# Kernel optimization log

Measured on AMD Instinct MI355X. Metric: run time of the kernel, lower is better.

The kernel has to match this reference:

```python
import jax, jax.numpy as jnp
import numpy as np

N = 50000      # nodes
E = 800000     # edges (before self-loops)
IN = 128       # in_channels
HID = 16       # hidden_channels
HEADS = 8
OUT = 16       # out_channels
NEG_SLOPE = 0.2
BN_EPS = 1e-5
LN_EPS = 1e-5


def setup_inputs() -> dict:
    key = jax.random.key(0)
    ks = jax.random.split(key, 16)
    s = 0.05
    inp = {
        "x": jax.random.normal(ks[0], (N, IN), jnp.float32),
        "edge_index": jax.random.randint(ks[1], (2, E), 0, N, jnp.int64),
        # conv1 (in=IN, out=HID, heads=HEADS, concat=True)
        "Wl1": jax.random.normal(ks[2], (HEADS * HID, IN), jnp.float32) * s,
        "bl1": jnp.zeros((HEADS * HID,), jnp.float32),
        "Wr1": jax.random.normal(ks[3], (HEADS * HID, IN), jnp.float32) * s,
        "br1": jnp.zeros((HEADS * HID,), jnp.float32),
        "att1": jax.random.normal(ks[4], (HEADS, HID), jnp.float32) * s,
        "bias1": jnp.zeros((HEADS * HID,), jnp.float32),
        # batchnorm (eval mode, running stats)
        "bn_w": jnp.ones((HEADS * HID,), jnp.float32),
        "bn_b": jnp.zeros((HEADS * HID,), jnp.float32),
        "bn_rm": jnp.zeros((HEADS * HID,), jnp.float32),
        "bn_rv": jnp.ones((HEADS * HID,), jnp.float32),
        # conv2 (in=HEADS*HID, out=OUT, heads=HEADS, concat=False)
        "Wl2": jax.random.normal(ks[5], (HEADS * OUT, HEADS * HID), jnp.float32) * s,
        "bl2": jnp.zeros((HEADS * OUT,), jnp.float32),
        "Wr2": jax.random.normal(ks[6], (HEADS * OUT, HEADS * HID), jnp.float32) * s,
        "br2": jnp.zeros((HEADS * OUT,), jnp.float32),
        "att2": jax.random.normal(ks[7], (HEADS, OUT), jnp.float32) * s,
        "bias2": jnp.zeros((OUT,), jnp.float32),
        # skip + layernorm
        "Wskip": jax.random.normal(ks[8], (OUT, IN), jnp.float32) * s,
        "ln_w": jnp.ones((OUT,), jnp.float32),
        "ln_b": jnp.zeros((OUT,), jnp.float32),
    }
    return inp


def _gatv2(x, src, dst, Wl, bl, Wr, br, att, bias, heads, ch, concat):
    """PyG GATv2Conv (share_weights=False), eval mode (no dropout)."""
    n = x.shape[0]
    xl = (x @ Wl.T + bl).reshape(n, heads, ch)   # source transform
    xr = (x @ Wr.T + br).reshape(n, heads, ch)   # target transform
    # edge-wise attention score
    e = jax.nn.leaky_relu(xl[src] + xr[dst], NEG_SLOPE)          # [E',H,C]
    score = jnp.einsum('ehc,hc->eh', e, att)                      # [E',H]
    # segment softmax over incoming edges per destination node
    smax = jax.ops.segment_max(score, dst, num_segments=n)
    ex = jnp.exp(score - smax[dst])
    denom = jax.ops.segment_sum(ex, dst, num_segments=n)
    alpha = ex / denom[dst]                                       # [E',H]
    out = jax.ops.segment_sum(alpha[:, :, None] * xl[src], dst, num_segments=n)
    if concat:
        out = out.reshape(n, heads * ch)
    else:
        out = out.mean(axis=1)
    return out + bias


def reference(x, edge_index, Wl1, bl1, Wr1, br1, att1, bias1,
              bn_w, bn_b, bn_rm, bn_rv,
              Wl2, bl2, Wr2, br2, att2, bias2,
              Wskip, ln_w, ln_b):
    n = x.shape[0]
    loops = jnp.arange(n, dtype=edge_index.dtype)
    src = jnp.concatenate([edge_index[0], loops])
    dst = jnp.concatenate([edge_index[1], loops])

    x_res = x @ Wskip.T                                            # [N,OUT]

    h = _gatv2(x, src, dst, Wl1, bl1, Wr1, br1, att1, bias1, HEADS, HID, True)
    # BatchNorm1d in eval mode
    h = (h - bn_rm) * jax.lax.rsqrt(bn_rv + BN_EPS) * bn_w + bn_b
    h = jax.nn.elu(h)

    h = _gatv2(h, src, dst, Wl2, bl2, Wr2, br2, att2, bias2, HEADS, OUT, False)

    y = h + x_res
    mu = y.mean(axis=-1, keepdims=True)
    var = ((y - mu) ** 2).mean(axis=-1, keepdims=True)
    return (y - mu) * jax.lax.rsqrt(var + LN_EPS) * ln_w + ln_b
```

## Files before the change

### kernel.cpp

```cpp
#include <hip/hip_runtime.h>

#define NEG_SLOPE 0.2f
#define BN_EPS 1e-5f
#define LN_EPS 1e-5f

#if __has_builtin(__builtin_amdgcn_exp2f)
#define EXP2F(x) __builtin_amdgcn_exp2f(x)
#else
#define EXP2F(x) exp2f(x)
#endif

typedef __bf16 bf16_t;
typedef bf16_t bf16x8 __attribute__((ext_vector_type(8)));
typedef float floatx4 __attribute__((ext_vector_type(4)));

__device__ __forceinline__ unsigned short f2bf(float f) {
  unsigned u = __float_as_uint(f);
  u += 0x7FFFu + ((u >> 16) & 1u);
  return (unsigned short)(u >> 16);
}
__device__ __forceinline__ float bf_lo(unsigned u) { return __uint_as_float(u << 16); }
__device__ __forceinline__ float bf_hi(unsigned u) { return __uint_as_float(u & 0xFFFF0000u); }

__global__ void cvt_all(const float* __restrict__ wl1, const float* __restrict__ wr1,
                        const float* __restrict__ wl2, const float* __restrict__ wr2,
                        const float* __restrict__ wsk,
                        const float* __restrict__ bias1,
                        const float* __restrict__ bn_w, const float* __restrict__ bn_b,
                        const float* __restrict__ bn_rm, const float* __restrict__ bn_rv,
                        const int* __restrict__ ei, int E,
                        unsigned short* __restrict__ wcat1,
                        unsigned short* __restrict__ wcat2,
                        int* __restrict__ deg8, unsigned short* __restrict__ rpos,
                        float* __restrict__ bnS, float* __restrict__ bnT,
                        int N) {
  const int W4 = 128 * 128 / 4;
  const int S4 = 16 * 128 / 4;
  int j = blockIdx.x * blockDim.x + threadIdx.x;
  const float* src;
  unsigned short* dst;
  if (j < W4)               { src = wl1; dst = wcat1; }
  else if (j < 2 * W4)      { src = wr1; dst = wcat1 + 128 * 128; j -= W4; }
  else if (j < 3 * W4)      { src = wl2; dst = wcat2; j -= 2 * W4; }
  else if (j < 4 * W4)      { src = wr2; dst = wcat2 + 128 * 128; j -= 3 * W4; }
  else if (j < 4 * W4 + S4) { src = wsk; dst = wcat1 + 256 * 128; j -= 4 * W4; }
  else {
    j -= 4 * W4 + S4;
    if (j < 32) {
      for (int t = j * 4; t < j * 4 + 4; ++t) {
        float S = bn_w[t] * rsqrtf(bn_rv[t] + BN_EPS);
        bnS[t] = S;
        bnT[t] = (bias1[t] - bn_rm[t]) * S + bn_b[t];
      }
    } else {
      int e = j - 32;
      if (e < E) {
        int d = ei[E + e];
        int c = (int)(blockIdx.x & 7);
        rpos[e] = (unsigned short)atomicAdd(&deg8[(size_t)c * N + d], 1);
      }
    }
    return;
  }
  float4 v = ((const float4*)src)[j];
  ushort4 o;
  o.x = f2bf(v.x); o.y = f2bf(v.y); o.z = f2bf(v.z); o.w = f2bf(v.w);
  ((ushort4*)dst)[j] = o;
}

__global__ __launch_bounds__(1024)
void csr_scan(const int* __restrict__ deg8, int* __restrict__ meta,
              int* __restrict__ cbase8, int* bsum, int N) {
  __shared__ int wsum[16];
  __shared__ int sh_base;
  int b = blockIdx.x;
  int tid = threadIdx.x;
  int lane = tid & 63, wid = tid >> 6;
  int i0 = b * 4096 + tid * 4;

  int4 v[8];
#pragma unroll
  for (int c = 0; c < 8; ++c) {
    const int* p = deg8 + (size_t)c * N;
    v[c] = make_int4(0, 0, 0, 0);
    if (i0 + 3 < N) v[c] = *(const int4*)(p + i0);
    else if (i0 < N) {
      v[c].x = p[i0];
      if (i0 + 1 < N) v[c].y = p[i0 + 1];
      if (i0 + 2 < N) v[c].z = p[i0 + 2];
    }
  }
  int4 run = make_int4(0, 0, 0, 0);
#pragma unroll
  for (int c = 0; c < 8; ++c) {
    int4 t = v[c];
    v[c] = run;
    run.x += t.x; run.y += t.y; run.z += t.z; run.w += t.w;
  }
  int g1 = (run.x + 1) & ~1, g2 = (run.y + 1) & ~1, g3 = (run.z + 1) & ~1, g4 = (run.w + 1) & ~1;
  int s1 = g1, s2 = s1 + g2, s3 = s2 + g3, s4 = s3 + g4;
  int s = s4;
#pragma unroll
  for (int d = 1; d < 64; d <<= 1) { int t = __shfl_up(s, d, 64); if (lane >= d) s += t; }
  if (lane == 63) wsum[wid] = s;
  __syncthreads();
  if (tid < 16) {
    int ws = wsum[tid];
#pragma unroll
    for (int d = 1; d < 16; d <<= 1) { int t = __shfl_up(ws, d, 16); if (tid >= d) ws += t; }
    wsum[tid] = ws;
  }
  __syncthreads();
  if (tid == 0) {
    __hip_atomic_store(&bsum[b], wsum[15] + 1, __ATOMIC_RELEASE, __HIP_MEMORY_SCOPE_AGENT);
    int base = 0;
    for (int j = 0; j < b; ++j) {
      int x;
      do { x = __hip_atomic_load(&bsum[j], __ATOMIC_ACQUIRE, __HIP_MEMORY_SCOPE_AGENT); } while (x == 0);
      base += x - 1;
    }
    sh_base = base;
  }
  __syncthreads();
  int off = sh_base + (wid ? wsum[wid - 1] : 0) + (s - s4);
  int st[4] = {off, off + s1, off + s2, off + s3};
  int tv[4] = {run.x, run.y, run.z, run.w};
#pragma unroll
  for (int k = 0; k < 4; ++k)
    if (i0 + k < N) ((int2*)meta)[i0 + k] = make_int2(st[k], tv[k]);
#pragma unroll
  for (int c = 0; c < 8; ++c) {
    int* p = cbase8 + (size_t)c * N;
    if (i0 + 3 < N) {
      *(int4*)(p + i0) = make_int4(st[0] + v[c].x, st[1] + v[c].y, st[2] + v[c].z, st[3] + v[c].w);
    } else if (i0 < N) {
      p[i0] = st[0] + v[c].x;
      if (i0 + 1 < N) p[i0 + 1] = st[1] + v[c].y;
      if (i0 + 2 < N) p[i0 + 2] = st[2] + v[c].z;
    }
  }
}

template <bool MIXED, bool AF32>
__device__ __forceinline__ void gemm_body(int wv, int lane,
    const void* __restrict__ Av, const unsigned short* __restrict__ B,
    const float* __restrict__ bias0, const float* __restrict__ bias1,
    unsigned short* __restrict__ Cbf, float* __restrict__ Cf, int M, int pstrips) {
  int mtiles = (M + 31) >> 5;
  if (wv >= mtiles * 2) return;
  int mt = wv >> 1, sub = wv & 1;
  int r = lane & 15, quad = lane >> 4;

  bf16x8 a0[4], a1[4];
  if (AF32) {
    const float* Af = (const float*)Av;
    int r0 = min(mt * 32 + r, M - 1);
    int r1 = min(mt * 32 + 16 + r, M - 1);
    const float* A0 = Af + (size_t)r0 * 128 + quad * 8;
    const float* A1 = Af + (size_t)r1 * 128 + quad * 8;
#pragma unroll
    for (int k = 0; k < 4; ++k) {
      float4 fa = *(const float4*)(A0 + 32 * k);
      float4 fb = *(const float4*)(A0 + 32 * k + 4);
      float4 ga = *(const float4*)(A1 + 32 * k);
      float4 gb = *(const float4*)(A1 + 32 * k + 4);
      union { bf16x8 v; unsigned short s[8]; } t0, t1;
      t0.s[0] = f2bf(fa.x); t0.s[1] = f2bf(fa.y); t0.s[2] = f2bf(fa.z); t0.s[3] = f2bf(fa.w);
      t0.s[4] = f2bf(fb.x); t0.s[5] = f2bf(fb.y); t0.s[6] = f2bf(fb.z); t0.s[7] = f2bf(fb.w);
      t1.s[0] = f2bf(ga.x); t1.s[1] = f2bf(ga.y); t1.s[2] = f2bf(ga.z); t1.s[3] = f2bf(ga.w);
      t1.s[4] = f2bf(gb.x); t1.s[5] = f2bf(gb.y); t1.s[6] = f2bf(gb.z); t1.s[7] = f2bf(gb.w);
      a0[k] = t0.v;
      a1[k] = t1.v;
    }
  } else {
    const unsigned short* Au = (const unsigned short*)Av;
    const unsigned short* Abase = Au + (size_t)(mt * 32 + r) * 128 + quad * 8;
#pragma unroll
    for (int k = 0; k < 4; ++k) {
      a0[k] = *(const bf16x8*)(Abase + 32 * k);
      a1[k] = *(const bf16x8*)(Abase + 16 * 128 + 32 * k);
    }
  }

  int row0 = mt * 32 + quad * 4;
  const int Ptot = MIXED ? 272 : 256;
  for (int ps = sub; ps < pstrips; ps += 2) {
#pragma unroll
    for (int pp = 0; pp < 4; ++pp) {
      int p0 = ps * 64 + pp * 16;
      if (p0 >= Ptot) break;
      const unsigned short* Bbase = B + (size_t)(p0 + r) * 128 + quad * 8;
      bf16x8 b[4];
#pragma unroll
      for (int k = 0; k < 4; ++k) b[k] = *(const bf16x8*)(Bbase + 32 * k);
      floatx4 acc0 = {0.f, 0.f, 0.f, 0.f};
      floatx4 acc1 = {0.f, 0.f, 0.f, 0.f};
#pragma unroll
      for (int k = 0; k < 4; ++k) {
        acc0 = __builtin_amdgcn_mfma_f32_16x16x32_bf16(a0[k], b[k], acc0, 0, 0, 0);
        acc1 = __builtin_amdgcn_mfma_f32_16x16x32_bf16(a1[k], b[k], acc1, 0, 0, 0);
      }
      int col = p0 + r;
      if (MIXED && col >= 256) {
#pragma unroll
        for (int i = 0; i < 4; ++i) {
          if (row0 + i < M)      Cf[(size_t)(row0 + i) * 16 + (col - 256)] = acc0[i];
          if (row0 + 16 + i < M) Cf[(size_t)(row0 + 16 + i) * 16 + (col - 256)] = acc1[i];
        }
      } else {
        float bs = (col < 128) ? bias0[col] : bias1[col - 128];
#pragma unroll
        for (int i = 0; i < 4; ++i) {
          if (row0 + i < M)      Cbf[(size_t)(row0 + i) * 256 + col] = f2bf(acc0[i] + bs);
          if (row0 + 16 + i < M) Cbf[(size_t)(row0 + 16 + i) * 256 + col] = f2bf(acc1[i] + bs);
        }
      }
    }
  }
}

__global__ __launch_bounds__(256)
void gemm_bf16_mfma(const unsigned short* __restrict__ A, const unsigned short* __restrict__ B,
                    const float* __restrict__ bias0, const float* __restrict__ bias1,
                    unsigned short* __restrict__ Cbf, float* __restrict__ Cf,
                    int M, int pstrips) {
  gemm_body<false, false>((int)((blockIdx.x * blockDim.x + threadIdx.x) >> 6),
                          (int)(threadIdx.x & 63), A, B, bias0, bias1, Cbf, Cf, M, pstrips);
}

__global__ __launch_bounds__(256)
void gemm1_scatter(const float* __restrict__ A, const unsigned short* __restrict__ B,
                   const float* __restrict__ bias0, const float* __restrict__ bias1,
                   unsigned short* __restrict__ Cbf, float* __restrict__ Cf,
                   int M, int pstrips, int gemmBlocks,
                   const int* __restrict__ ei, int E, int ebase,
                   const int* __restrict__ cbase8, const unsigned short* __restrict__ rpos,
                   unsigned short* __restrict__ csr, int N) {
  if ((int)blockIdx.x >= gemmBlocks) {
    int e = ((int)blockIdx.x - gemmBlocks) * 256 + (int)threadIdx.x;
    if (e < E) {
      int d = ei[E + e];
      int c = ((ebase + e) >> 8) & 7;
      csr[cbase8[(size_t)c * N + d] + (int)rpos[e]] = (unsigned short)ei[e];
    }
    return;
  }
  gemm_body<true, true>((int)((blockIdx.x * blockDim.x + threadIdx.x) >> 6),
                        (int)(threadIdx.x & 63), A, B, bias0, bias1, Cbf, Cf, M, pstrips);
}

template <int LAYER>
__global__ __launch_bounds__(256)
void gat_agg(const unsigned int* __restrict__ xlr,
             const int* __restrict__ meta,
             const unsigned short* __restrict__ csr,
             const float* __restrict__ att,
             const float* __restrict__ p0, const float* __restrict__ p1,
             const float* __restrict__ p2, const float* __restrict__ p3,
             void* __restrict__ outp, int n, int nwaves) {
  int lane = threadIdx.x & 63;
  int gw = (int)((blockIdx.x * blockDim.x + threadIdx.x) >> 6);
  int slot = lane >> 4;
  int sl4 = lane & 15;
  const char* __restrict__ xb = (const char*)xlr;
  const unsigned slOff = (unsigned)(sl4 << 4);
  const int hsh = (slot & 1) << 4;
  const bool whi = (slot >= 2);
  float4 atA = ((const float4*)att)[sl4 * 2];
  float4 atB = ((const float4*)att)[sl4 * 2 + 1];
  const float SC = 0.6f * 1.44269504f;
  float a0 = SC * atA.x, a1 = SC * atA.y, a2 = SC * atA.z, a3 = SC * atA.w;
  float a4 = SC * atB.x, a5 = SC * atB.y, a6 = SC * atB.z, a7 = SC * atB.w;

  for (int dst = gw; dst < n; dst += nwaves) {
    int dsts = __builtin_amdgcn_readfirstlane(dst);
    int2 m = *(const int2*)(meta + 2 * (size_t)dsts);
    int beg = __builtin_amdgcn_readfirstlane(m.x);
    int dg  = __builtin_amdgcn_readfirstlane(m.y);
    const unsigned* cp = (const unsigned*)csr + (beg >> 1);

    uint4 urw = *(const uint4*)(xb + (((unsigned)dsts << 9) + 256u + slOff));
    float xr0 = bf_lo(urw.x), xr1 = bf_hi(urw.x), xr2 = bf_lo(urw.y), xr3 = bf_hi(urw.y);
    float xr4 = bf_lo(urw.z), xr5 = bf_hi(urw.z), xr6 = bf_lo(urw.w), xr7 = bf_hi(urw.w);

    float l = 0.f;
    float c0 = 0.f, c1 = 0.f, c2 = 0.f, c3 = 0.f;
    float c4 = 0.f, c5 = 0.f, c6 = 0.f, c7 = 0.f;

    auto gat = [&](unsigned w0, unsigned w1) -> uint4 {
      unsigned pr = whi ? w1 : w0;
      unsigned s = (pr >> hsh) & 0xFFFFu;
      return *(const uint4*)(xb + ((s << 9) + slOff));
    };

    auto body = [&](uint4 u, float vm, bool masked) {
      float x0 = bf_lo(u.x), x1 = bf_hi(u.x), x2 = bf_lo(u.y), x3 = bf_hi(u.y);
      float x4 = bf_lo(u.z), x5 = bf_hi(u.z), x6 = bf_lo(u.w), x7 = bf_hi(u.w);
      float e0 = x0 + xr0, e1 = x1 + xr1, e2 = x2 + xr2, e3 = x3 + xr3;
      float e4 = x4 + xr4, e5 = x5 + xr5, e6 = x6 + xr6, e7 = x7 + xr7;
      float sc = fmaf(fmaf(fabsf(e0), 0.66666667f, e0), a0,
                 fmaf(fmaf(fabsf(e1), 0.66666667f, e1), a1,
                 fmaf(fmaf(fabsf(e2), 0.66666667f, e2), a2,
                 fmaf(fmaf(fabsf(e3), 0.66666667f, e3), a3,
                 fmaf(fmaf(fabsf(e4), 0.66666667f, e4), a4,
                 fmaf(fmaf(fabsf(e5), 0.66666667f, e5), a5,
                 fmaf(fmaf(fabsf(e6), 0.66666667f, e6), a6,
                      fmaf(fabsf(e7), 0.66666667f, e7) * a7)))))));
      sc += __shfl_xor(sc, 1);
      float pw = EXP2F(sc);
      if (masked) pw *= vm;
      l += pw;
      c0 = fmaf(pw, x0, c0); c1 = fmaf(pw, x1, c1);
      c2 = fmaf(pw, x2, c2); c3 = fmaf(pw, x3, c3);
      c4 = fmaf(pw, x4, c4); c5 = fmaf(pw, x5, c5);
      c6 = fmaf(pw, x6, c6); c7 = fmaf(pw, x7, c7);
    };

    int nq = dg >> 2;
    int q = 0;
    int nq4 = nq & ~3;
    for (; q < nq4; q += 4) {
      unsigned w[8];
#pragma unroll
      for (int k = 0; k < 8; ++k) w[k] = cp[2 * q + k];
      uint4 u[4];
#pragma unroll
      for (int k = 0; k < 4; ++k) u[k] = gat(w[2 * k], w[2 * k + 1]);
#pragma unroll
      for (int k = 0; k < 4; ++k) body(u[k], 1.f, false);
    }
    if (nq - q >= 2) {
      unsigned w[4];
#pragma unroll
      for (int k = 0; k < 4; ++k) w[k] = cp[2 * q + k];
      uint4 u[2];
#pragma unroll
      for (int k = 0; k < 2; ++k) u[k] = gat(w[2 * k], w[2 * k + 1]);
#pragma unroll
      for (int k = 0; k < 2; ++k) body(u[k], 1.f, false);
      q += 2;
    }
    if (nq - q >= 1) {
      unsigned w0 = cp[2 * q], w1 = cp[2 * q + 1];
      body(gat(w0, w1), 1.f, false);
      q += 1;
    }
    {
      unsigned w0 = cp[2 * q], w1 = cp[2 * q + 1];
      int tot = dg + 1;
      int e = 4 * q + slot;
      unsigned pr = whi ? w1 : w0;
      unsigned sE = (pr >> hsh) & 0xFFFFu;
      unsigned s = (e < dg) ? sE : (unsigned)dsts;
      float vm = (e < tot) ? 1.f : 0.f;
      uint4 u = *(const uint4*)(xb + ((s << 9) + slOff));
      body(u, vm, true);
    }

    l  += __shfl_xor(l, 16);  l  += __shfl_xor(l, 32);
    c0 += __shfl_xor(c0, 16); c0 += __shfl_xor(c0, 32);
    c1 += __shfl_xor(c1, 16); c1 += __shfl_xor(c1, 32);
    c2 += __shfl_xor(c2, 16); c2 += __shfl_xor(c2, 32);
    c3 += __shfl_xor(c3, 16); c3 += __shfl_xor(c3, 32);
    c4 += __shfl_xor(c4, 16); c4 += __shfl_xor(c4, 32);
    c5 += __shfl_xor(c5, 16); c5 += __shfl_xor(c5, 32);
    c6 += __shfl_xor(c6, 16); c6 += __shfl_xor(c6, 32);
    c7 += __shfl_xor(c7, 16); c7 += __shfl_xor(c7, 32);
    float inv = 1.f / l;

    if (LAYER == 1) {
      float4 Sa = *(const float4*)(p0 + sl4 * 8);
      float4 Sb = *(const float4*)(p0 + sl4 * 8 + 4);
      float4 Ta = *(const float4*)(p1 + sl4 * 8);
      float4 Tb = *(const float4*)(p1 + sl4 * 8 + 4);
      float o0 = fmaf(c0 * inv, Sa.x, Ta.x);
      float o1 = fmaf(c1 * inv, Sa.y, Ta.y);
      float o2 = fmaf(c2 * inv, Sa.z, Ta.z);
      float o3 = fmaf(c3 * inv, Sa.w, Ta.w);
      float o4 = fmaf(c4 * inv, Sb.x, Tb.x);
      float o5 = fmaf(c5 * inv, Sb.y, Tb.y);
      float o6 = fmaf(c6 * inv, Sb.z, Tb.z);
      float o7 = fmaf(c7 * inv, Sb.w, Tb.w);
      o0 = (o0 > 0.f) ? o0 : (__expf(o0) - 1.f);
      o1 = (o1 > 0.f) ? o1 : (__expf(o1) - 1.f);
      o2 = (o2 > 0.f) ? o2 : (__expf(o2) - 1.f);
      o3 = (o3 > 0.f) ? o3 : (__expf(o3) - 1.f);
      o4 = (o4 > 0.f) ? o4 : (__expf(o4) - 1.f);
      o5 = (o5 > 0.f) ? o5 : (__expf(o5) - 1.f);
      o6 = (o6 > 0.f) ? o6 : (__expf(o6) - 1.f);
      o7 = (o7 > 0.f) ? o7 : (__expf(o7) - 1.f);
      if (slot == 0) {
        uint4 o;
        o.x = ((unsigned)f2bf(o1) << 16) | f2bf(o0);
        o.y = ((unsigned)f2bf(o3) << 16) | f2bf(o2);
        o.z = ((unsigned)f2bf(o5) << 16) | f2bf(o4);
        o.w = ((unsigned)f2bf(o7) << 16) | f2bf(o6);
        ((uint4*)outp)[(size_t)dsts * 16 + sl4] = o;
      }
    } else {
      float y0 = c0 * inv, y1 = c1 * inv, y2 = c2 * inv, y3 = c3 * inv;
      float y4 = c4 * inv, y5 = c5 * inv, y6 = c6 * inv, y7 = c7 * inv;
#pragma unroll
      for (int d = 2; d <= 8; d <<= 1) {
        y0 += __shfl_xor(y0, d); y1 += __shfl_xor(y1, d);
        y2 += __shfl_xor(y2, d); y3 += __shfl_xor(y3, d);
        y4 += __shfl_xor(y4, d); y5 += __shfl_xor(y5, d);
        y6 += __shfl_xor(y6, d); y7 += __shfl_xor(y7, d);
      }
      int chh = (sl4 & 1) * 8;
      float4 b2a = *(const float4*)(p1 + chh);
      float4 b2b = *(const float4*)(p1 + chh + 4);
      float4 xsa = *(const float4*)(p0 + (size_t)dsts * 16 + chh);
      float4 xsb = *(const float4*)(p0 + (size_t)dsts * 16 + chh + 4);
      y0 = y0 * 0.125f + b2a.x + xsa.x;
      y1 = y1 * 0.125f + b2a.y + xsa.y;
      y2 = y2 * 0.125f + b2a.z + xsa.z;
      y3 = y3 * 0.125f + b2a.w + xsa.w;
      y4 = y4 * 0.125f + b2b.x + xsb.x;
      y5 = y5 * 0.125f + b2b.y + xsb.y;
      y6 = y6 * 0.125f + b2b.z + xsb.z;
      y7 = y7 * 0.125f + b2b.w + xsb.w;
      float t = ((y0 + y1) + (y2 + y3)) + ((y4 + y5) + (y6 + y7));
      t += __shfl_xor(t, 1);
      float mu = t * (1.f / 16.f);
      float d0 = y0 - mu, d1 = y1 - mu, d2 = y2 - mu, d3 = y3 - mu;
      float d4 = y4 - mu, d5 = y5 - mu, d6 = y6 - mu, d7 = y7 - mu;
      float v = ((d0 * d0 + d1 * d1) + (d2 * d2 + d3 * d3)) +
                ((d4 * d4 + d5 * d5) + (d6 * d6 + d7 * d7));
      v += __shfl_xor(v, 1);
      float istd = rsqrtf(v * (1.f / 16.f) + LN_EPS);
      float4 lwa = *(const float4*)(p2 + chh);
      float4 lwb = *(const float4*)(p2 + chh + 4);
      float4 lba = *(const float4*)(p3 + chh);
      float4 lbb = *(const float4*)(p3 + chh + 4);
      if (lane < 2) {
        float4 oa, ob;
        oa.x = d0 * istd * lwa.x + lba.x;
        oa.y = d1 * istd * lwa.y + lba.y;
        oa.z = d2 * istd * lwa.z + lba.z;
        oa.w = d3 * istd * lwa.w + lba.w;
        ob.x = d4 * istd * lwb.x + lbb.x;
        ob.y = d5 * istd * lwb.y + lbb.y;
        ob.z = d6 * istd * lwb.z + lbb.z;
        ob.w = d7 * istd * lwb.w + lbb.w;
        float* op = (float*)outp + (size_t)dsts * 16 + chh;
        *(float4*)op = oa;
        *(float4*)(op + 4) = ob;
      }
    }
  }
}

extern "C" void kernel_launch(void* const* d_in, const int* in_sizes, int n_in,
                              void* d_out, int out_size, void* d_ws, size_t ws_size,
                              hipStream_t stream) {
  const float* x     = (const float*)d_in[0];
  const int*   ei    = (const int*)d_in[1];
  const float* Wl1   = (const float*)d_in[2];
  const float* bl1   = (const float*)d_in[3];
  const float* Wr1   = (const float*)d_in[4];
  const float* br1   = (const float*)d_in[5];
  const float* att1  = (const float*)d_in[6];
  const float* bias1 = (const float*)d_in[7];
  const float* bn_w  = (const float*)d_in[8];
  const float* bn_b  = (const float*)d_in[9];
  const float* bn_rm = (const float*)d_in[10];
  const float* bn_rv = (const float*)d_in[11];
  const float* Wl2   = (const float*)d_in[12];
  const float* bl2   = (const float*)d_in[13];
  const float* Wr2   = (const float*)d_in[14];
  const float* br2   = (const float*)d_in[15];
  const float* att2  = (const float*)d_in[16];
  const float* bias2 = (const float*)d_in[17];
  const float* Wskip = (const float*)d_in[18];
  const float* ln_w  = (const float*)d_in[19];
  const float* ln_b  = (const float*)d_in[20];

  const int N = in_sizes[0] / 128;
  const int E = in_sizes[1] / 2;

  char* w = (char*)d_ws;
  size_t off = 0;
  auto alloc = [&](size_t bytes) -> void* {
    void* p = (void*)(w + off);
    off += (bytes + 255) & ~(size_t)255;
    return p;
  };
  unsigned short* wcat1  = (unsigned short*)alloc(272 * 128 * 2);
  unsigned short* wcat2  = (unsigned short*)alloc(256 * 128 * 2);
  unsigned int*   xlr    = (unsigned int*)alloc((size_t)N * 128 * 4);
  float*          xres   = (float*)alloc((size_t)N * 16 * 4);
  unsigned short* hbf    = (unsigned short*)alloc((size_t)N * 128 * 2);
  float*          bnS    = (float*)alloc(128 * 4);
  float*          bnT    = (float*)alloc(128 * 4);
  int*            deg8   = (int*)alloc((size_t)8 * N * 4);
  int*            bsum   = (int*)alloc(64 * 4);
  int*            cbase8 = (int*)alloc((size_t)8 * N * 4);
  int*            meta   = (int*)alloc((size_t)2 * N * 4);
  unsigned short* rpos   = (unsigned short*)alloc((size_t)E * 2);
  unsigned short* csr    = (unsigned short*)alloc((size_t)(E + N) * 2 + 256);

  const int W4 = 128 * 128 / 4, S4 = 16 * 128 / 4;
  const int ebase = 4 * W4 + S4 + 32;
  const int nb = (N + 4095) / 4096;

  hipMemsetAsync(deg8, 0, (size_t)8 * N * 4 + 256 + 64 * 4, stream);
  {
    int tot = ebase + E;
    cvt_all<<<(tot + 255) / 256, 256, 0, stream>>>(
        Wl1, Wr1, Wl2, Wr2, Wskip, bias1, bn_w, bn_b, bn_rm, bn_rv, ei, E,
        wcat1, wcat2, deg8, rpos, bnS, bnT, N);
  }

  csr_scan<<<nb, 1024, 0, stream>>>(deg8, meta, cbase8, bsum, N);

  {
    int mtiles = (N + 31) >> 5;
    int waves = mtiles * 2;
    int gemmBlocks = (waves + 3) / 4;
    int scatBlocks = (E + 255) / 256;
    gemm1_scatter<<<gemmBlocks + scatBlocks, 256, 0, stream>>>(
        x, wcat1, bl1, br1, (unsigned short*)xlr, xres, N, 5, gemmBlocks,
        ei, E, ebase, cbase8, rpos, csr, N);
  }

  {
    int blocks = 6144, nwaves = blocks * 4;
    gat_agg<1><<<blocks, 256, 0, stream>>>(xlr, meta, csr, att1,
                                           bnS, bnT, nullptr, nullptr, (void*)hbf, N, nwaves);
  }

  {
    int mtiles = (N + 31) >> 5;
    int waves = mtiles * 2;
    gemm_bf16_mfma<<<(waves + 3) / 4, 256, 0, stream>>>(
        hbf, wcat2, bl2, br2, (unsigned short*)xlr, nullptr, N, 4);
  }

  {
    int blocks = 6144, nwaves = blocks * 4;
    gat_agg<2><<<blocks, 256, 0, stream>>>(xlr, meta, csr, att2,
                                           xres, bias2, ln_w, ln_b, d_out, N, nwaves);
  }
}
```

Measured before the change: 301.3 us.

## Split interleaved xl/xr buffer into separate arrays and shrink aggregation grid

The GEMM outputs for the source (xl) and target (xr) transforms move out of one interleaved 512-byte-per-node row into two separate 256-byte-per-node arrays. The aggregation kernels gather only xl rows, so the gathered table is denser, which should make better use of cache. The aggregation launch also drops from 6144 to 2048 blocks, so each wave handles more destination nodes in its grid-stride loop.

```diff
diff --git a/kernel.cpp b/kernel.cpp
--- a/kernel.cpp
+++ b/kernel.cpp
@@ -145,7 +145,8 @@
 __device__ __forceinline__ void gemm_body(int wv, int lane,
     const void* __restrict__ Av, const unsigned short* __restrict__ B,
     const float* __restrict__ bias0, const float* __restrict__ bias1,
-    unsigned short* __restrict__ Cbf, float* __restrict__ Cf, int M, int pstrips) {
+    unsigned short* __restrict__ Cl, unsigned short* __restrict__ Cr,
+    float* __restrict__ Cf, int M, int pstrips) {
   int mtiles = (M + 31) >> 5;
   if (wv >= mtiles * 2) return;
   int mt = wv >> 1, sub = wv & 1;
@@ -209,10 +210,12 @@
         }
       } else {
         float bs = (col < 128) ? bias0[col] : bias1[col - 128];
+        unsigned short* Ct = (col < 128) ? Cl : Cr;
+        int cc = col & 127;
 #pragma unroll
         for (int i = 0; i < 4; ++i) {
-          if (row0 + i < M)      Cbf[(size_t)(row0 + i) * 256 + col] = f2bf(acc0[i] + bs);
-          if (row0 + 16 + i < M) Cbf[(size_t)(row0 + 16 + i) * 256 + col] = f2bf(acc1[i] + bs);
+          if (row0 + i < M)      Ct[(size_t)(row0 + i) * 128 + cc] = f2bf(acc0[i] + bs);
+          if (row0 + 16 + i < M) Ct[(size_t)(row0 + 16 + i) * 128 + cc] = f2bf(acc1[i] + bs);
         }
       }
     }
@@ -222,16 +225,18 @@
 __global__ __launch_bounds__(256)
 void gemm_bf16_mfma(const unsigned short* __restrict__ A, const unsigned short* __restrict__ B,
                     const float* __restrict__ bias0, const float* __restrict__ bias1,
-                    unsigned short* __restrict__ Cbf, float* __restrict__ Cf,
+                    unsigned short* __restrict__ Cl, unsigned short* __restrict__ Cr,
                     int M, int pstrips) {
   gemm_body<false, false>((int)((blockIdx.x * blockDim.x + threadIdx.x) >> 6),
-                          (int)(threadIdx.x & 63), A, B, bias0, bias1, Cbf, Cf, M, pstrips);
+                          (int)(threadIdx.x & 63), A, B, bias0, bias1, Cl, Cr, nullptr,
+                          M, pstrips);
 }
 
 __global__ __launch_bounds__(256)
 void gemm1_scatter(const float* __restrict__ A, const unsigned short* __restrict__ B,
                    const float* __restrict__ bias0, const float* __restrict__ bias1,
-                   unsigned short* __restrict__ Cbf, float* __restrict__ Cf,
+                   unsigned short* __restrict__ Cl, unsigned short* __restrict__ Cr,
+                   float* __restrict__ Cf,
                    int M, int pstrips, int gemmBlocks,
                    const int* __restrict__ ei, int E, int ebase,
                    const int* __restrict__ cbase8, const unsigned short* __restrict__ rpos,
@@ -246,12 +251,13 @@
     return;
   }
   gemm_body<true, true>((int)((blockIdx.x * blockDim.x + threadIdx.x) >> 6),
-                        (int)(threadIdx.x & 63), A, B, bias0, bias1, Cbf, Cf, M, pstrips);
+                        (int)(threadIdx.x & 63), A, B, bias0, bias1, Cl, Cr, Cf, M, pstrips);
 }
 
 template <int LAYER>
 __global__ __launch_bounds__(256)
-void gat_agg(const unsigned int* __restrict__ xlr,
+void gat_agg(const unsigned short* __restrict__ xlt,
+             const unsigned short* __restrict__ xrt,
              const int* __restrict__ meta,
              const unsigned short* __restrict__ csr,
              const float* __restrict__ att,
@@ -262,7 +268,7 @@
   int gw = (int)((blockIdx.x * blockDim.x + threadIdx.x) >> 6);
   int slot = lane >> 4;
   int sl4 = lane & 15;
-  const char* __restrict__ xb = (const char*)xlr;
+  const char* __restrict__ xb = (const char*)xlt;
   const unsigned slOff = (unsigned)(sl4 << 4);
   const int hsh = (slot & 1) << 4;
   const bool whi = (slot >= 2);
@@ -279,7 +285,7 @@
     int dg  = __builtin_amdgcn_readfirstlane(m.y);
     const unsigned* cp = (const unsigned*)csr + (beg >> 1);
 
-    uint4 urw = *(const uint4*)(xb + (((unsigned)dsts << 9) + 256u + slOff));
+    uint4 urw = *(const uint4*)((const char*)xrt + (((unsigned)dsts << 8) + slOff));
     float xr0 = bf_lo(urw.x), xr1 = bf_hi(urw.x), xr2 = bf_lo(urw.y), xr3 = bf_hi(urw.y);
     float xr4 = bf_lo(urw.z), xr5 = bf_hi(urw.z), xr6 = bf_lo(urw.w), xr7 = bf_hi(urw.w);
 
@@ -290,7 +296,7 @@
     auto gat = [&](unsigned w0, unsigned w1) -> uint4 {
       unsigned pr = whi ? w1 : w0;
       unsigned s = (pr >> hsh) & 0xFFFFu;
-      return *(const uint4*)(xb + ((s << 9) + slOff));
+      return *(const uint4*)(xb + ((s << 8) + slOff));
     };
 
     auto body = [&](uint4 u, float vm, bool masked) {
@@ -353,7 +359,7 @@
       unsigned sE = (pr >> hsh) & 0xFFFFu;
       unsigned s = (e < dg) ? sE : (unsigned)dsts;
       float vm = (e < tot) ? 1.f : 0.f;
-      uint4 u = *(const uint4*)(xb + ((s << 9) + slOff));
+      uint4 u = *(const uint4*)(xb + ((s << 8) + slOff));
       body(u, vm, true);
     }
 
@@ -488,7 +494,8 @@
   };
   unsigned short* wcat1  = (unsigned short*)alloc(272 * 128 * 2);
   unsigned short* wcat2  = (unsigned short*)alloc(256 * 128 * 2);
-  unsigned int*   xlr    = (unsigned int*)alloc((size_t)N * 128 * 4);
+  unsigned short* xlt    = (unsigned short*)alloc((size_t)N * 128 * 2);
+  unsigned short* xrt    = (unsigned short*)alloc((size_t)N * 128 * 2);
   float*          xres   = (float*)alloc((size_t)N * 16 * 4);
   unsigned short* hbf    = (unsigned short*)alloc((size_t)N * 128 * 2);
   float*          bnS    = (float*)alloc(128 * 4);
@@ -520,13 +527,13 @@
     int gemmBlocks = (waves + 3) / 4;
     int scatBlocks = (E + 255) / 256;
     gemm1_scatter<<<gemmBlocks + scatBlocks, 256, 0, stream>>>(
-        x, wcat1, bl1, br1, (unsigned short*)xlr, xres, N, 5, gemmBlocks,
+        x, wcat1, bl1, br1, xlt, xrt, xres, N, 5, gemmBlocks,
         ei, E, ebase, cbase8, rpos, csr, N);
   }
 
   {
-    int blocks = 6144, nwaves = blocks * 4;
-    gat_agg<1><<<blocks, 256, 0, stream>>>(xlr, meta, csr, att1,
+    int blocks = 2048, nwaves = blocks * 4;
+    gat_agg<1><<<blocks, 256, 0, stream>>>(xlt, xrt, meta, csr, att1,
                                            bnS, bnT, nullptr, nullptr, (void*)hbf, N, nwaves);
   }
 
@@ -534,12 +541,12 @@
     int mtiles = (N + 31) >> 5;
     int waves = mtiles * 2;
     gemm_bf16_mfma<<<(waves + 3) / 4, 256, 0, stream>>>(
-        hbf, wcat2, bl2, br2, (unsigned short*)xlr, nullptr, N, 4);
+        hbf, wcat2, bl2, br2, xlt, xrt, N, 4);
   }
 
   {
-    int blocks = 6144, nwaves = blocks * 4;
-    gat_agg<2><<<blocks, 256, 0, stream>>>(xlr, meta, csr, att2,
+    int blocks = 2048, nwaves = blocks * 4;
+    gat_agg<2><<<blocks, 256, 0, stream>>>(xlt, xrt, meta, csr, att2,
                                            xres, bias2, ln_w, ln_b, d_out, N, nwaves);
   }
 }
```

After: 298.3 us. No clear change (-1.0%).
